# Kernel optimization log

Hardware: AMD Instinct MI355X
Metric: run time of the kernel (lower is better)

Reference implementation:

```python
import jax, jax.numpy as jnp
import numpy as np

EMBED_DIM = 1024
NUM_HEADS = 16
HEAD_DIM = EMBED_DIM // NUM_HEADS
SCALE = float(np.sqrt(HEAD_DIM))
B, TQ, TK = 2, 2048, 2048


def setup_inputs() -> dict:
    key = jax.random.key(0)
    ks = jax.random.split(key, 16)
    s = 1.0 / np.sqrt(EMBED_DIM)
    inp = {
        "query": jax.random.normal(ks[0], (B, TQ, EMBED_DIM), jnp.float32),
        "key": jax.random.normal(ks[1], (B, TK, EMBED_DIM), jnp.float32),
        "value": jax.random.normal(ks[2], (B, TK, EMBED_DIM), jnp.float32),
        "key_padding_mask": jnp.zeros((B, TK), dtype=bool),
        "Wq": jax.random.uniform(ks[3], (EMBED_DIM, EMBED_DIM), jnp.float32, -s, s),
        "bq": jax.random.uniform(ks[4], (EMBED_DIM,), jnp.float32, -s, s),
        "Wk": jax.random.uniform(ks[5], (EMBED_DIM, EMBED_DIM), jnp.float32, -s, s),
        "bk": jax.random.uniform(ks[6], (EMBED_DIM,), jnp.float32, -s, s),
        "Wv": jax.random.uniform(ks[7], (EMBED_DIM, EMBED_DIM), jnp.float32, -s, s),
        "bv": jax.random.uniform(ks[8], (EMBED_DIM,), jnp.float32, -s, s),
        "Wo": jax.random.uniform(ks[9], (EMBED_DIM, EMBED_DIM), jnp.float32, -s, s),
        "bo": jax.random.uniform(ks[10], (EMBED_DIM,), jnp.float32, -s, s),
        "clr_bias_q": jax.random.normal(ks[11], (NUM_HEADS, 1, HEAD_DIM), jnp.float32) * 0.02,
        "clr_bias_k": jax.random.normal(ks[12], (NUM_HEADS, 1, HEAD_DIM), jnp.float32) * 0.02,
    }
    return inp


def reference(query, key, value, key_padding_mask, Wq, bq, Wk, bk, Wv, bv, Wo, bo,
              clr_bias_q, clr_bias_k):
    Bsz, Tq, _ = query.shape
    Tk = key.shape[1]

    def split_heads(x, W, b, T):
        # Linear (torch convention: x @ W.T + b) then [B, H, T, Dh]
        y = jnp.einsum('bte,fe->btf', x, W) + b
        return y.reshape(Bsz, T, NUM_HEADS, HEAD_DIM).transpose(0, 2, 1, 3)

    q = split_heads(query, Wq, bq, Tq)   # [B,H,Tq,Dh]
    k = split_heads(key, Wk, bk, Tk)     # [B,H,Tk,Dh]
    v = split_heads(value, Wv, bv, Tk)   # [B,H,Tk,Dh]

    # CLR centering + learned bias (Aitchison similarity)
    q_c = q - jnp.mean(q, axis=-1, keepdims=True) + clr_bias_q[None]
    k_c = k - jnp.mean(k, axis=-1, keepdims=True) + clr_bias_k[None]
    scores = jnp.einsum('bhqd,bhkd->bhqk', q_c, k_c) / SCALE  # [B,H,Tq,Tk]

    mask = key_padding_mask[:, None, None, :]  # [B,1,1,Tk], True = ignore
    scores = jnp.where(mask, -jnp.inf, scores)

    attn = jax.nn.softmax(scores, axis=-1)
    out = jnp.einsum('bhqk,bhkd->bhqd', attn, v)
    out = out.transpose(0, 2, 1, 3).reshape(Bsz, Tq, EMBED_DIM)
    return jnp.einsum('bte,fe->btf', out, Wo) + bo
```

## Files before the change

### kernel.cpp

```cpp
#include <hip/hip_runtime.h>
#include <stdint.h>

static constexpr int EMB   = 1024;
static constexpr int HEADS = 16;
static constexpr int HD    = 64;
static constexpr int BATCH = 2;
static constexpr int SEQ   = 2048;
static constexpr int BT    = BATCH * SEQ;
static constexpr float QSC = 0.18033688011112042f;

typedef short   short8  __attribute__((ext_vector_type(8)));
typedef float   float4v __attribute__((ext_vector_type(4)));

__device__ __forceinline__ ushort f2bf(float f) {
    union { float f; uint32_t i; } v; v.f = f;
    uint32_t x = v.i;
    return (ushort)((x + 0x7FFFu + ((x >> 16) & 1u)) >> 16);
}
__device__ __forceinline__ uint32_t pack2bf(float lo, float hi) {
    union { float f; uint32_t u; } a, b; a.f = lo; b.f = hi;
    uint32_t ra = a.u + 0x7FFFu + ((a.u >> 16) & 1u);
    uint32_t rb = b.u + 0x7FFFu + ((b.u >> 16) & 1u);
    return (rb & 0xFFFF0000u) | (ra >> 16);
}

__device__ __forceinline__ void async_ld16(const void* g, void* l) {
    __builtin_amdgcn_global_load_lds(
        (const __attribute__((address_space(1))) void*)g,
        (__attribute__((address_space(3))) void*)l,
        16, 0, 0);
}

__global__ void cvt_all(const float* __restrict__ q, const float* __restrict__ k,
                        const float* __restrict__ v,
                        const float* __restrict__ wq, const float* __restrict__ wk,
                        const float* __restrict__ wv, const float* __restrict__ wo,
                        ushort* __restrict__ qb, ushort* __restrict__ kb,
                        ushort* __restrict__ vb,
                        ushort* __restrict__ wqb, ushort* __restrict__ wkb,
                        ushort* __restrict__ wvb, ushort* __restrict__ wob)
{
    int bid = blockIdx.x;
    const float* src; ushort* dst; size_t off;
    if (bid < 6144) {
        int seg = bid >> 11;
        src = seg == 0 ? q : (seg == 1 ? k : v);
        dst = seg == 0 ? qb : (seg == 1 ? kb : vb);
        off = (size_t)(bid & 2047) * 2048;
    } else {
        int t = bid - 6144, seg = t >> 9;
        src = seg == 0 ? wq : (seg == 1 ? wk : (seg == 2 ? wv : wo));
        dst = seg == 0 ? wqb : (seg == 1 ? wkb : (seg == 2 ? wvb : wob));
        off = (size_t)(t & 511) * 2048;
    }
    size_t base = off + (size_t)threadIdx.x * 8;
    float4 a0 = *(const float4*)(src + base);
    float4 a1 = *(const float4*)(src + base + 4);
    uint32_t o[4] = { pack2bf(a0.x, a0.y), pack2bf(a0.z, a0.w),
                      pack2bf(a1.x, a1.y), pack2bf(a1.z, a1.w) };
    *(uint4*)(dst + base) = *(uint4*)o;
}

template<int MODE>
__global__ __launch_bounds__(256, 2)
void gemm_bt(const ushort* __restrict__ A, const ushort* __restrict__ W,
             const float* __restrict__ bias, const float* __restrict__ clrb,
             float scale,
             float* __restrict__ Yf, ushort* __restrict__ Yb,
             int M, int N, int K)
{
    __shared__ __align__(16) ushort As[64 * 64];
    __shared__ __align__(16) ushort Ws[128 * 64];

    const int tid  = threadIdx.x;
    const int wid  = tid >> 6;
    const int lane = tid & 63;
    const int m0 = blockIdx.y * 64;
    const int n0 = blockIdx.x * 128;
    const int wm = (wid >> 1) * 32;
    const int wn = (wid & 1) * 64;

    float4v acc[2][4];
#pragma unroll
    for (int i = 0; i < 2; i++)
#pragma unroll
        for (int j = 0; j < 4; j++) acc[i][j] = (float4v)0.0f;

    const int lrow8 = lane >> 3;
    const int gcA   = (lane & 7) ^ lrow8;
    const ushort* Ab = A + (size_t)m0 * K + gcA * 8;
    const ushort* Wb = W + (size_t)n0 * K + gcA * 8;

    for (int k0 = 0; k0 < K; k0 += 64) {
        __syncthreads();
#pragma unroll
        for (int it = 0; it < 2; ++it) {
            int row = (it * 4 + wid) * 8 + lrow8;
            async_ld16(Ab + (size_t)row * K + k0, &As[(it * 4 + wid) * 512]);
        }
#pragma unroll
        for (int it = 0; it < 4; ++it) {
            int row = (it * 4 + wid) * 8 + lrow8;
            async_ld16(Wb + (size_t)row * K + k0, &Ws[(it * 4 + wid) * 512]);
        }
        __syncthreads();
#pragma unroll
        for (int ks = 0; ks < 2; ++ks) {
            const int c = ks * 4 + (lane >> 4);
            short8 af[2], wf[4];
#pragma unroll
            for (int i = 0; i < 2; i++) {
                int row = wm + i * 16 + (lane & 15);
                af[i] = *(const short8*)&As[row * 64 + ((c ^ (row & 7)) * 8)];
            }
#pragma unroll
            for (int j = 0; j < 4; j++) {
                int row = wn + j * 16 + (lane & 15);
                wf[j] = *(const short8*)&Ws[row * 64 + ((c ^ (row & 7)) * 8)];
            }
#pragma unroll
            for (int i = 0; i < 2; i++)
#pragma unroll
                for (int j = 0; j < 4; j++)
                    acc[i][j] = __builtin_amdgcn_mfma_f32_16x16x32_bf16(af[i], wf[j], acc[i][j], 0, 0, 0);
        }
    }

    const int h = (n0 + wn) >> 6;
#pragma unroll
    for (int i = 0; i < 2; i++) {
        float ys[4][4];
#pragma unroll
        for (int j = 0; j < 4; j++) {
            float bj = bias[n0 + wn + j * 16 + (lane & 15)];
#pragma unroll
            for (int r = 0; r < 4; r++) ys[j][r] = acc[i][j][r] + bj;
        }
        const int rowb = m0 + wm + i * 16 + ((lane >> 4) << 2);

        if constexpr (MODE == 0) {
#pragma unroll
            for (int j = 0; j < 4; j++) {
                int col = n0 + wn + j * 16 + (lane & 15);
#pragma unroll
                for (int r = 0; r < 4; r++)
                    Yf[(size_t)(rowb + r) * N + col] = ys[j][r];
            }
        } else if constexpr (MODE == 1) {
            float rs[4];
#pragma unroll
            for (int r = 0; r < 4; r++)
                rs[r] = ys[0][r] + ys[1][r] + ys[2][r] + ys[3][r];
#pragma unroll
            for (int r = 0; r < 4; r++)
#pragma unroll
                for (int off = 1; off < 16; off <<= 1)
                    rs[r] += __shfl_xor(rs[r], off, 64);
#pragma unroll
            for (int j = 0; j < 4; j++) {
                int d = j * 16 + (lane & 15);
                float cb = clrb[h * HD + d];
#pragma unroll
                for (int r = 0; r < 4; r++) {
                    int row = rowb + r;
                    int b = row >> 11, t = row & (SEQ - 1);
                    Yb[((size_t)(b * HEADS + h) * SEQ + t) * HD + d] =
                        f2bf((ys[j][r] - rs[r] * (1.0f / 64.0f) + cb) * scale);
                }
            }
        } else {
#pragma unroll
            for (int j = 0; j < 4; j++) {
                int d = j * 16 + (lane & 15);
#pragma unroll
                for (int r = 0; r < 4; r++) {
                    int row = rowb + r;
                    int b = row >> 11, t = row & (SEQ - 1);
                    Yb[((size_t)(b * HEADS + h) * HD + d) * SEQ + t] = f2bf(ys[j][r]);
                }
            }
        }
    }
}

__global__ __launch_bounds__(256, 2)
void attn_kernel(const ushort* __restrict__ qc,
                 const ushort* __restrict__ kc,
                 const ushort* __restrict__ vt,
                 const unsigned char* __restrict__ mask,
                 ushort* __restrict__ out)
{
    __shared__ __align__(16) ushort Ks[128 * 64];
    __shared__ __align__(16) ushort Vs[64 * 128];
    __shared__ __align__(16) ushort Ps[4][16 * 136];

    const int tid  = threadIdx.x;
    const int wid  = tid >> 6;
    const int lane = tid & 63;

    const int bid = blockIdx.x;
    const int qt = bid & 31;
    const int h  = (bid >> 5) & 15;
    const int b  = bid >> 9;

    const ushort* qbase = qc + ((size_t)(b * HEADS + h)) * SEQ * HD;
    const ushort* kbase = kc + ((size_t)(b * HEADS + h)) * SEQ * HD;
    const ushort* vbase = vt + ((size_t)(b * HEADS + h)) * HD * SEQ;

    const int qrow = qt * 64 + wid * 16 + (lane & 15);
    short8 qf[2];
#pragma unroll
    for (int ks = 0; ks < 2; ++ks)
        qf[ks] = *(const short8*)(qbase + (size_t)qrow * HD + ks * 32 + (lane >> 4) * 8);

    float l_r[4] = {0.f, 0.f, 0.f, 0.f};
    float4v o[4];
#pragma unroll
    for (int j = 0; j < 4; j++) o[j] = (float4v)0.f;

    const int lrow8 = lane >> 3;
    const int gcK   = (lane & 7) ^ lrow8;
    ushort* Pw = &Ps[wid][0];

    for (int kt = 0; kt < SEQ / 128; ++kt) {
        __syncthreads();
#pragma unroll
        for (int it = 0; it < 4; ++it) {
            int row = (it * 4 + wid) * 8 + lrow8;
            async_ld16(kbase + (size_t)(kt * 128 + row) * HD + gcK * 8,
                       &Ks[(it * 4 + wid) * 512]);
        }
#pragma unroll
        for (int it = 0; it < 4; ++it) {
            int row = (it * 4 + wid) * 4 + (lane >> 4);
            int gc  = (lane & 15) ^ (row & 15);
            async_ld16(vbase + (size_t)row * SEQ + kt * 128 + gc * 8,
                       &Vs[(it * 4 + wid) * 512]);
        }
        __syncthreads();

        float4v s[8];
#pragma unroll
        for (int j = 0; j < 8; j++) {
            s[j] = (float4v)0.f;
#pragma unroll
            for (int ks = 0; ks < 2; ks++) {
                int row = j * 16 + (lane & 15);
                int c   = ks * 4 + (lane >> 4);
                short8 kf = *(const short8*)&Ks[row * 64 + ((c ^ (row & 7)) * 8)];
                s[j] = __builtin_amdgcn_mfma_f32_16x16x32_bf16(qf[ks], kf, s[j], 0, 0, 0);
            }
        }

#pragma unroll
        for (int j = 0; j < 8; j++) {
            int key = kt * 128 + j * 16 + (lane & 15);
            bool mk = mask[b * SEQ + key] != 0;
            int prow = ((lane >> 4) << 2) * 136 + j * 16 + (lane & 15);
#pragma unroll
            for (int r = 0; r < 4; r++) {
                float p = exp2f(mk ? -1e30f : s[j][r]);
                l_r[r] += p;
                Pw[prow + r * 136] = f2bf(p);
            }
        }
        asm volatile("s_waitcnt lgkmcnt(0)" ::: "memory");

        short8 pf[4];
#pragma unroll
        for (int ks = 0; ks < 4; ks++)
            pf[ks] = *(const short8*)&Pw[(lane & 15) * 136 + ks * 32 + (lane >> 4) * 8];

#pragma unroll
        for (int j = 0; j < 4; j++) {
            int d = j * 16 + (lane & 15);
#pragma unroll
            for (int ks = 0; ks < 4; ks++) {
                int c = ks * 4 + (lane >> 4);
                short8 vf = *(const short8*)&Vs[d * 128 + ((c ^ (d & 15)) * 8)];
                o[j] = __builtin_amdgcn_mfma_f32_16x16x32_bf16(pf[ks], vf, o[j], 0, 0, 0);
            }
        }
    }

#pragma unroll
    for (int r = 0; r < 4; r++)
#pragma unroll
        for (int off = 1; off < 16; off <<= 1)
            l_r[r] += __shfl_xor(l_r[r], off, 64);

    const int qrow_out = qt * 64 + wid * 16 + ((lane >> 4) << 2);
#pragma unroll
    for (int j = 0; j < 4; j++) {
        int d = j * 16 + (lane & 15);
#pragma unroll
        for (int r = 0; r < 4; r++) {
            float val = o[j][r] / l_r[r];
            out[((size_t)(b * SEQ + qrow_out + r)) * EMB + h * HD + d] = f2bf(val);
        }
    }
}

extern "C" void kernel_launch(void* const* d_in, const int* in_sizes, int n_in,
                              void* d_out, int out_size, void* d_ws, size_t ws_size,
                              hipStream_t stream)
{
    const float* query = (const float*)d_in[0];
    const float* key_  = (const float*)d_in[1];
    const float* value = (const float*)d_in[2];
    const unsigned char* mask = (const unsigned char*)d_in[3];
    const float* Wq  = (const float*)d_in[4];
    const float* bq  = (const float*)d_in[5];
    const float* Wk  = (const float*)d_in[6];
    const float* bk  = (const float*)d_in[7];
    const float* Wv  = (const float*)d_in[8];
    const float* bv  = (const float*)d_in[9];
    const float* Wo  = (const float*)d_in[10];
    const float* bo  = (const float*)d_in[11];
    const float* cbq = (const float*)d_in[12];
    const float* cbk = (const float*)d_in[13];

    ushort* ws = (ushort*)d_ws;
    const size_t n1 = (size_t)BT * EMB;
    const size_t nw = (size_t)EMB * EMB;
    ushort* qb  = ws;
    ushort* kb  = qb  + n1;
    ushort* vb  = kb  + n1;
    ushort* wqb = vb  + n1;
    ushort* wkb = wqb + nw;
    ushort* wvb = wkb + nw;
    ushort* wob = wvb + nw;
    ushort* qc  = wob + nw;
    ushort* kc  = qc  + n1;
    ushort* vt  = kc  + n1;
    ushort* ao  = qb;

    cvt_all<<<8192, 256, 0, stream>>>(query, key_, value, Wq, Wk, Wv, Wo,
                                      qb, kb, vb, wqb, wkb, wvb, wob);

    dim3 gg(EMB / 128, BT / 64);
    gemm_bt<1><<<gg, 256, 0, stream>>>(qb, wqb, bq, cbq, QSC, nullptr, qc, BT, EMB, EMB);
    gemm_bt<1><<<gg, 256, 0, stream>>>(kb, wkb, bk, cbk, 1.0f, nullptr, kc, BT, EMB, EMB);
    gemm_bt<2><<<gg, 256, 0, stream>>>(vb, wvb, bv, nullptr, 1.0f, nullptr, vt, BT, EMB, EMB);

    attn_kernel<<<BATCH * HEADS * (SEQ / 64), 256, 0, stream>>>(qc, kc, vt, mask, ao);

    gemm_bt<0><<<gg, 256, 0, stream>>>(ao, wob, bo, nullptr, 1.0f, (float*)d_out, nullptr, BT, EMB, EMB);
}
```

Before: 276.3 us.

## Use 128x128 GEMM tiles and batch Q/K/V projections into one launch

Raises the GEMM block tile from 64x128 to 128x128, with each warp computing a 64x64 sub-tile. This improves operand reuse from shared memory and cuts global loads per FLOP. The three Q/K/V projection GEMMs are merged into a single launch using blockIdx.z, which removes launch overhead and gives one larger grid. The trade-off is that the larger accumulator array raises register pressure and the grid holds fewer blocks, which may reduce occupancy and wave balance, especially for the output GEMM.

Result: faster. 265.0 us (-4.1%).

```diff
diff --git a/kernel.cpp b/kernel.cpp
--- a/kernel.cpp
+++ b/kernel.cpp
@@ -61,74 +61,92 @@
     *(uint4*)(dst + base) = *(uint4*)o;
 }
 
-template<int MODE>
+__device__ __forceinline__ void gemm_core_128(
+    const ushort* __restrict__ A, const ushort* __restrict__ W,
+    int m0, int n0, int K,
+    ushort* As, ushort* Ws,
+    int wid, int lane, float4v acc[4][4])
+{
+    const int lrow8 = lane >> 3;
+    const int gc    = (lane & 7) ^ lrow8;
+    const ushort* Ab = A + (size_t)m0 * K + gc * 8;
+    const ushort* Wb = W + (size_t)n0 * K + gc * 8;
+    const int wm = (wid >> 1) * 64;
+    const int wn = (wid & 1) * 64;
+
+    for (int k0 = 0; k0 < K; k0 += 64) {
+        __syncthreads();
+#pragma unroll
+        for (int it = 0; it < 4; ++it) {
+            int rg = it * 4 + wid;
+            int row = rg * 8 + lrow8;
+            async_ld16(Ab + (size_t)row * K + k0, &As[rg * 512]);
+            async_ld16(Wb + (size_t)row * K + k0, &Ws[rg * 512]);
+        }
+        __syncthreads();
+#pragma unroll
+        for (int ks = 0; ks < 2; ++ks) {
+            const int c = ks * 4 + (lane >> 4);
+            short8 af[4], wf[4];
+#pragma unroll
+            for (int i = 0; i < 4; i++) {
+                int row = wm + i * 16 + (lane & 15);
+                af[i] = *(const short8*)&As[row * 64 + ((c ^ (row & 7)) * 8)];
+            }
+#pragma unroll
+            for (int j = 0; j < 4; j++) {
+                int row = wn + j * 16 + (lane & 15);
+                wf[j] = *(const short8*)&Ws[row * 64 + ((c ^ (row & 7)) * 8)];
+            }
+#pragma unroll
+            for (int i = 0; i < 4; i++)
+#pragma unroll
+                for (int j = 0; j < 4; j++)
+                    acc[i][j] = __builtin_amdgcn_mfma_f32_16x16x32_bf16(af[i], wf[j], acc[i][j], 0, 0, 0);
+        }
+    }
+}
+
 __global__ __launch_bounds__(256, 2)
-void gemm_bt(const ushort* __restrict__ A, const ushort* __restrict__ W,
-             const float* __restrict__ bias, const float* __restrict__ clrb,
-             float scale,
-             float* __restrict__ Yf, ushort* __restrict__ Yb,
-             int M, int N, int K)
-{
-    __shared__ __align__(16) ushort As[64 * 64];
+void gemm_qkv(const ushort* __restrict__ qb, const ushort* __restrict__ kb,
+              const ushort* __restrict__ vb,
+              const ushort* __restrict__ wqb, const ushort* __restrict__ wkb,
+              const ushort* __restrict__ wvb,
+              const float* __restrict__ bq, const float* __restrict__ bk,
+              const float* __restrict__ bv,
+              const float* __restrict__ cbq, const float* __restrict__ cbk,
+              ushort* __restrict__ qc, ushort* __restrict__ kc,
+              ushort* __restrict__ vt)
+{
+    __shared__ __align__(16) ushort As[128 * 64];
     __shared__ __align__(16) ushort Ws[128 * 64];
+
+    const int z = blockIdx.z;
+    const ushort* A    = z == 0 ? qb  : (z == 1 ? kb  : vb);
+    const ushort* W    = z == 0 ? wqb : (z == 1 ? wkb : wvb);
+    const float*  bias = z == 0 ? bq  : (z == 1 ? bk  : bv);
+    const float*  clrb = z == 0 ? cbq : cbk;
+    const float   scale = z == 0 ? QSC : 1.0f;
 
     const int tid  = threadIdx.x;
     const int wid  = tid >> 6;
     const int lane = tid & 63;
-    const int m0 = blockIdx.y * 64;
+    const int m0 = blockIdx.y * 128;
     const int n0 = blockIdx.x * 128;
-    const int wm = (wid >> 1) * 32;
+    const int wm = (wid >> 1) * 64;
     const int wn = (wid & 1) * 64;
 
-    float4v acc[2][4];
-#pragma unroll
-    for (int i = 0; i < 2; i++)
+    float4v acc[4][4];
+#pragma unroll
+    for (int i = 0; i < 4; i++)
 #pragma unroll
         for (int j = 0; j < 4; j++) acc[i][j] = (float4v)0.0f;
 
-    const int lrow8 = lane >> 3;
-    const int gcA   = (lane & 7) ^ lrow8;
-    const ushort* Ab = A + (size_t)m0 * K + gcA * 8;
-    const ushort* Wb = W + (size_t)n0 * K + gcA * 8;
-
-    for (int k0 = 0; k0 < K; k0 += 64) {
-        __syncthreads();
-#pragma unroll
-        for (int it = 0; it < 2; ++it) {
-            int row = (it * 4 + wid) * 8 + lrow8;
-            async_ld16(Ab + (size_t)row * K + k0, &As[(it * 4 + wid) * 512]);
-        }
-#pragma unroll
-        for (int it = 0; it < 4; ++it) {
-            int row = (it * 4 + wid) * 8 + lrow8;
-            async_ld16(Wb + (size_t)row * K + k0, &Ws[(it * 4 + wid) * 512]);
-        }
-        __syncthreads();
-#pragma unroll
-        for (int ks = 0; ks < 2; ++ks) {
-            const int c = ks * 4 + (lane >> 4);
-            short8 af[2], wf[4];
-#pragma unroll
-            for (int i = 0; i < 2; i++) {
-                int row = wm + i * 16 + (lane & 15);
-                af[i] = *(const short8*)&As[row * 64 + ((c ^ (row & 7)) * 8)];
-            }
-#pragma unroll
-            for (int j = 0; j < 4; j++) {
-                int row = wn + j * 16 + (lane & 15);
-                wf[j] = *(const short8*)&Ws[row * 64 + ((c ^ (row & 7)) * 8)];
-            }
-#pragma unroll
-            for (int i = 0; i < 2; i++)
-#pragma unroll
-                for (int j = 0; j < 4; j++)
-                    acc[i][j] = __builtin_amdgcn_mfma_f32_16x16x32_bf16(af[i], wf[j], acc[i][j], 0, 0, 0);
-        }
-    }
+    gemm_core_128(A, W, m0, n0, EMB, As, Ws, wid, lane, acc);
 
     const int h = (n0 + wn) >> 6;
 #pragma unroll
-    for (int i = 0; i < 2; i++) {
+    for (int i = 0; i < 4; i++) {
         float ys[4][4];
 #pragma unroll
         for (int j = 0; j < 4; j++) {
@@ -138,15 +156,7 @@
         }
         const int rowb = m0 + wm + i * 16 + ((lane >> 4) << 2);
 
-        if constexpr (MODE == 0) {
-#pragma unroll
-            for (int j = 0; j < 4; j++) {
-                int col = n0 + wn + j * 16 + (lane & 15);
-#pragma unroll
-                for (int r = 0; r < 4; r++)
-                    Yf[(size_t)(rowb + r) * N + col] = ys[j][r];
-            }
-        } else if constexpr (MODE == 1) {
+        if (z < 2) {
             float rs[4];
 #pragma unroll
             for (int r = 0; r < 4; r++)
@@ -156,6 +166,7 @@
 #pragma unroll
                 for (int off = 1; off < 16; off <<= 1)
                     rs[r] += __shfl_xor(rs[r], off, 64);
+            ushort* Yb = z == 0 ? qc : kc;
 #pragma unroll
             for (int j = 0; j < 4; j++) {
                 int d = j * 16 + (lane & 15);
@@ -176,9 +187,46 @@
                 for (int r = 0; r < 4; r++) {
                     int row = rowb + r;
                     int b = row >> 11, t = row & (SEQ - 1);
-                    Yb[((size_t)(b * HEADS + h) * HD + d) * SEQ + t] = f2bf(ys[j][r]);
+                    vt[((size_t)(b * HEADS + h) * HD + d) * SEQ + t] = f2bf(ys[j][r]);
                 }
             }
+        }
+    }
+}
+
+__global__ __launch_bounds__(256, 2)
+void gemm_out(const ushort* __restrict__ A, const ushort* __restrict__ W,
+              const float* __restrict__ bias, float* __restrict__ Y)
+{
+    __shared__ __align__(16) ushort As[128 * 64];
+    __shared__ __align__(16) ushort Ws[128 * 64];
+
+    const int tid  = threadIdx.x;
+    const int wid  = tid >> 6;
+    const int lane = tid & 63;
+    const int m0 = blockIdx.y * 128;
+    const int n0 = blockIdx.x * 128;
+    const int wm = (wid >> 1) * 64;
+    const int wn = (wid & 1) * 64;
+
+    float4v acc[4][4];
+#pragma unroll
+    for (int i = 0; i < 4; i++)
+#pragma unroll
+        for (int j = 0; j < 4; j++) acc[i][j] = (float4v)0.0f;
+
+    gemm_core_128(A, W, m0, n0, EMB, As, Ws, wid, lane, acc);
+
+#pragma unroll
+    for (int i = 0; i < 4; i++) {
+        const int rowb = m0 + wm + i * 16 + ((lane >> 4) << 2);
+#pragma unroll
+        for (int j = 0; j < 4; j++) {
+            int col = n0 + wn + j * 16 + (lane & 15);
+            float bj = bias[col];
+#pragma unroll
+            for (int r = 0; r < 4; r++)
+                Y[(size_t)(rowb + r) * EMB + col] = acc[i][j][r] + bj;
         }
     }
 }
@@ -338,12 +386,12 @@
     cvt_all<<<8192, 256, 0, stream>>>(query, key_, value, Wq, Wk, Wv, Wo,
                                       qb, kb, vb, wqb, wkb, wvb, wob);
 
-    dim3 gg(EMB / 128, BT / 64);
-    gemm_bt<1><<<gg, 256, 0, stream>>>(qb, wqb, bq, cbq, QSC, nullptr, qc, BT, EMB, EMB);
-    gemm_bt<1><<<gg, 256, 0, stream>>>(kb, wkb, bk, cbk, 1.0f, nullptr, kc, BT, EMB, EMB);
-    gemm_bt<2><<<gg, 256, 0, stream>>>(vb, wvb, bv, nullptr, 1.0f, nullptr, vt, BT, EMB, EMB);
+    dim3 gq(EMB / 128, BT / 128, 3);
+    gemm_qkv<<<gq, 256, 0, stream>>>(qb, kb, vb, wqb, wkb, wvb,
+                                     bq, bk, bv, cbq, cbk, qc, kc, vt);
 
     attn_kernel<<<BATCH * HEADS * (SEQ / 64), 256, 0, stream>>>(qc, kc, vt, mask, ao);
 
-    gemm_bt<0><<<gg, 256, 0, stream>>>(ao, wob, bo, nullptr, 1.0f, (float*)d_out, nullptr, BT, EMB, EMB);
-}
+    dim3 go(EMB / 128, BT / 128);
+    gemm_out<<<go, 256, 0, stream>>>(ao, wob, bo, (float*)d_out);
+}
```
